# Kernel optimization log

Hardware: AMD Instinct MI355X
Metric: run time of the kernel (lower is better)

## Reference

```python
import jax, jax.numpy as jnp
import numpy as np

N_POL = 20000; N_COMP = 80000; N = N_POL + N_COMP
E = 1000000; EMB = 128; HID = 256; HEADS = 8; OUT = 128; EA = 5
NEG_SLOPE = 0.2; LN_EPS = 1e-5


def setup_inputs() -> dict:
    ks = jax.random.split(jax.random.key(0), 24)
    def rn(i, shape, s=0.1):
        return jax.random.normal(ks[i], shape, jnp.float32) * s
    C1 = HID // HEADS  # per-head channels of conv1
    return dict(
        pol_feat=rn(0, (N_POL, 7), 1.0),
        state_ids=jax.random.randint(ks[1], (N_POL,), 0, 55),
        comp_cat=jax.random.randint(ks[2], (N_COMP, 2), 0, 16),
        comp_price=rn(3, (N_COMP, 1), 1.0),
        edge_index=jax.random.randint(ks[4], (2, E), 0, N),
        edge_attr=rn(5, (E, EA), 1.0),
        Wp=rn(6, (7, EMB)), bp=jnp.zeros((EMB,), jnp.float32),
        state_emb=rn(7, (55, EMB)), sector_emb=rn(8, (16, 8)), industry_emb=rn(9, (150, 8)),
        Wc=rn(10, (17, EMB)), bc=jnp.zeros((EMB,), jnp.float32),
        ln_g=jnp.ones((EMB,), jnp.float32), ln_b=jnp.zeros((EMB,), jnp.float32),
        W1=rn(11, (EMB, HEADS * C1)), att_src1=rn(12, (HEADS, C1)), att_dst1=rn(13, (HEADS, C1)),
        We1=rn(14, (EA, HEADS * C1)), att_e1=rn(15, (HEADS, C1)), b1=jnp.zeros((HID,), jnp.float32),
        W2=rn(16, (HID, OUT)), att_src2=rn(17, (1, OUT)), att_dst2=rn(18, (1, OUT)),
        We2=rn(19, (EA, OUT)), att_e2=rn(20, (1, OUT)), b2=jnp.zeros((OUT,), jnp.float32),
    )


def _add_self_loops(src, dst, ea, n):
    # PyG add_self_loops with fill_value='mean': self-loop edge_attr = mean of
    # incoming edge attrs per dst node (0 for isolated nodes).
    loop = jnp.arange(n, dtype=src.dtype)
    cnt = jax.ops.segment_sum(jnp.ones(dst.shape, jnp.float32), dst, num_segments=n)
    loop_attr = jax.ops.segment_sum(ea, dst, num_segments=n) / jnp.maximum(cnt, 1.0)[:, None]
    return (jnp.concatenate([src, loop]), jnp.concatenate([dst, loop]),
            jnp.concatenate([ea, loop_attr], 0))


def _gat(x, src, dst, ea, W, a_src, a_dst, We, a_e, bias, concat):
    # PyG GATConv (shared lin for src/dst, edge_dim attention, eval mode).
    n = x.shape[0]
    H, C = a_src.shape
    xw = (x @ W).reshape(n, H, C)                 # [n,H,C]
    al_s = jnp.sum(xw * a_src, -1)                # [n,H]
    al_d = jnp.sum(xw * a_dst, -1)                # [n,H]
    ew = (ea @ We).reshape(-1, H, C)              # [Etot,H,C]
    al_e = jnp.sum(ew * a_e, -1)                  # [Etot,H]
    alpha = jax.nn.leaky_relu(al_s[src] + al_d[dst] + al_e, NEG_SLOPE)
    amax = jax.ops.segment_max(alpha, dst, num_segments=n)
    ex = jnp.exp(alpha - amax[dst])
    denom = jax.ops.segment_sum(ex, dst, num_segments=n)
    alpha = ex / (denom[dst] + 1e-16)             # segment softmax over dst
    out = jax.ops.segment_sum(xw[src] * alpha[:, :, None], dst, num_segments=n)
    out = out.reshape(n, H * C) if concat else out.mean(1)
    return out + bias


def reference(pol_feat, state_ids, comp_cat, comp_price, edge_index, edge_attr,
              Wp, bp, state_emb, sector_emb, industry_emb, Wc, bc, ln_g, ln_b,
              W1, att_src1, att_dst1, We1, att_e1, b1,
              W2, att_src2, att_dst2, We2, att_e2, b2):
    pol = jax.nn.relu(pol_feat @ Wp + bp) + state_emb[state_ids]
    comp_in = jnp.concatenate([sector_emb[comp_cat[:, 0]], industry_emb[comp_cat[:, 1]], comp_price], 1)
    comp = jax.nn.relu(comp_in @ Wc + bc)
    x = jnp.concatenate([pol, comp], 0)           # [N,EMB]
    mu = jnp.mean(x, -1, keepdims=True)
    var = jnp.var(x, -1, keepdims=True)
    x = (x - mu) / jnp.sqrt(var + LN_EPS) * ln_g + ln_b
    src, dst, ea = _add_self_loops(edge_index[0], edge_index[1], edge_attr, x.shape[0])
    h = jax.nn.elu(_gat(x, src, dst, ea, W1, att_src1, att_dst1, We1, att_e1, b1, True))
    return _gat(h, src, dst, ea, W2, att_src2, att_dst2, We2, att_e2, b2, False)
```

## Files before the change

### kernel.cpp

```cpp
#include <hip/hip_runtime.h>
#include <hip/hip_fp16.h>
#include <math.h>

#define N_POL 20000
#define N_COMP 80000
#define NN (N_POL + N_COMP)
#define EE 1000000
#define NB1 ((NN + 1023) / 1024)
#define LOG2E 1.44269504f
#define GB1 ((NN + 127) / 128)
#define SB ((EE + 255) / 256)
#define PB 341

typedef short bf16x8 __attribute__((ext_vector_type(8)));
typedef float f32x4 __attribute__((ext_vector_type(4)));

struct __align__(16) PEdge {
  int s;
  float ale2;
  unsigned short a1[8];
  unsigned pad[2];
};

__device__ __forceinline__ float wave_sum(float v) {
#pragma unroll
  for (int o = 32; o > 0; o >>= 1) v += __shfl_xor(v, o);
  return v;
}
__device__ __forceinline__ float wave_max(float v) {
#pragma unroll
  for (int o = 32; o > 0; o >>= 1) v = fmaxf(v, __shfl_xor(v, o));
  return v;
}
__device__ __forceinline__ unsigned short f2bf(float f) {
  unsigned b = __float_as_uint(f);
  return (unsigned short)((b + 0x7FFFu + ((b >> 16) & 1u)) >> 16);
}
__device__ __forceinline__ float bf2f(unsigned short u) {
  return __uint_as_float(((unsigned)u) << 16);
}
__device__ __forceinline__ unsigned short f2h(float f) {
  __half h = __float2half_rn(f);
  return *(unsigned short*)&h;
}
__device__ __forceinline__ float h2f(unsigned short u) {
  __half h = *(__half*)&u;
  return __half2float(h);
}

__global__ __launch_bounds__(256) void k_fuse1(
    const float* W1, const float* W2, const float* as2, const float* ad2,
    const float* We1, const float* ae1, const float* We2, const float* ae2,
    const float* sector_emb, const float* industry_emb, const float* Wc,
    const int* dst, unsigned short* W1t, unsigned short* W2t, float* Ts, float* Ti,
    float* us2, float* ud2, float* V1, float* V2, unsigned* hist) {
  int bid = blockIdx.x;
  if (bid >= PB) {
    int e = (bid - PB) * 256 + threadIdx.x;
    if (e < EE) atomicAdd(&hist[dst[e]], 1u);
    return;
  }
  int id = bid * 256 + threadIdx.x;
  if (id < 32768) {
    int n = id >> 7, k = id & 127;
    W1t[id] = f2bf(W1[k * 256 + n]);
  } else if (id < 65536) {
    int id2 = id - 32768;
    int n = id2 >> 8, k = id2 & 255;
    W2t[id2] = f2bf(W2[k * 128 + n]);
  } else if (id < 67584) {
    int id2 = id - 65536;
    int n = id2 >> 7, c = id2 & 127;
    float a = 0.f;
#pragma unroll
    for (int k = 0; k < 8; k++) a = fmaf(sector_emb[n * 8 + k], Wc[k * 128 + c], a);
    Ts[id2] = a;
  } else if (id < 86784) {
    int id2 = id - 67584;
    int n = id2 >> 7, c = id2 & 127;
    float a = 0.f;
#pragma unroll
    for (int k = 0; k < 8; k++) a = fmaf(industry_emb[n * 8 + k], Wc[(8 + k) * 128 + c], a);
    Ti[id2] = a;
  } else if (id < 87040) {
    int t = id - 86784;
    float s = 0.f, d = 0.f;
    for (int c = 0; c < 128; c++) {
      float w = W2[t * 128 + c];
      s = fmaf(w, as2[c], s);
      d = fmaf(w, ad2[c], d);
    }
    us2[t] = s * LOG2E;
    ud2[t] = d * LOG2E;
  } else if (id < 87104) {
    int t = id - 87040;
    int k = t >> 3, h = t & 7;
    if (k < 5) {
      float v = 0.f;
      for (int c = 0; c < 32; c++) v = fmaf(We1[k * 256 + h * 32 + c], ae1[h * 32 + c], v);
      V1[k * 8 + h] = v * LOG2E;
    }
  } else if (id < 87109) {
    int t = id - 87104;
    float v = 0.f;
    for (int c = 0; c < 128; c++) v = fmaf(We2[t * 128 + c], ae2[c], v);
    V2[t] = v * LOG2E;
  }
}

__global__ __launch_bounds__(256) void k_encode(
    const float* pol_feat, const int* state_ids, const int* comp_cat,
    const float* comp_price, const float* Wp, const float* bp, const float* state_emb,
    const float* Ts, const float* Ti, const float* Wc, const float* bc,
    const float* ln_g, const float* ln_b, unsigned short* x) {
  int t = threadIdx.x;
  int i = blockIdx.x * 2 + (t >> 7), c = t & 127;
  float v;
  if (i < N_POL) {
    float acc = bp[c];
#pragma unroll
    for (int k = 0; k < 7; k++) acc = fmaf(pol_feat[i * 7 + k], Wp[k * 128 + c], acc);
    v = fmaxf(acc, 0.f) + state_emb[state_ids[i] * 128 + c];
  } else {
    int j = i - N_POL;
    int sc = comp_cat[2 * j], in = comp_cat[2 * j + 1];
    float acc = Ts[sc * 128 + c] + Ti[in * 128 + c] +
                comp_price[j] * Wc[16 * 128 + c] + bc[c];
    v = fmaxf(acc, 0.f);
  }
  __shared__ float red[4];
  int wid = t >> 6, lane = t & 63;
  int base = (t >> 7) << 1;
  float s = wave_sum(v);
  if (lane == 0) red[wid] = s;
  __syncthreads();
  float mu = (red[base] + red[base + 1]) * (1.f / 128.f);
  float t0 = v - mu;
  __syncthreads();
  float s2 = wave_sum(t0 * t0);
  if (lane == 0) red[wid] = s2;
  __syncthreads();
  float var = (red[base] + red[base + 1]) * (1.f / 128.f);
  float r = rsqrtf(var + 1e-5f);
  float xf = t0 * r * ln_g[c] + ln_b[c];
  x[(size_t)i * 128 + c] = f2bf(xf);
}

__global__ __launch_bounds__(1024) void k_scan1(const unsigned* hist, unsigned* rowptr,
                                                unsigned* part) {
  __shared__ unsigned sc[1024];
  int t = threadIdx.x;
  int i = blockIdx.x * 1024 + t;
  unsigned v = (i < NN) ? hist[i] : 0u;
  sc[t] = v;
  __syncthreads();
  for (int o = 1; o < 1024; o <<= 1) {
    unsigned add = (t >= o) ? sc[t - o] : 0u;
    __syncthreads();
    sc[t] += add;
    __syncthreads();
  }
  if (i < NN) rowptr[i] = sc[t] - v;
  if (t == 1023) part[blockIdx.x] = sc[1023];
}
__global__ __launch_bounds__(256) void k_scan3(unsigned* rowptr, const unsigned* part,
                                               unsigned* cursor) {
  __shared__ unsigned pref[128];
  int t = threadIdx.x;
  unsigned orig = 0u;
  if (t < 128) {
    orig = (t < NB1) ? part[t] : 0u;
    pref[t] = orig;
  }
  __syncthreads();
  for (int o = 1; o < 128; o <<= 1) {
    unsigned add = 0u;
    if (t < 128 && t >= o) add = pref[t - o];
    __syncthreads();
    if (t < 128) pref[t] += add;
    __syncthreads();
  }
  if (t < 128) pref[t] -= orig;
  __syncthreads();
  int i = blockIdx.x * 256 + t;
  if (i < NN) {
    unsigned r = rowptr[i] + pref[i >> 10];
    rowptr[i] = r;
    cursor[i] = r;
  }
  if (i == 0) rowptr[NN] = EE;
}

__global__ __launch_bounds__(256) void k_fuse2(
    const unsigned short* x, const unsigned short* W1t, unsigned short* xw1,
    const int* src, const int* dst, const float* ea, const float* V1, const float* V2,
    unsigned* cursor, PEdge* ep) {
  __shared__ char wlds[65536];
  int bid = blockIdx.x;
  if (bid % 6 == 0) {
    int gb = bid / 6;
    int tid = threadIdx.x;
#pragma unroll
    for (int it = 0; it < 16; it++) {
      int cch = it * 256 + tid;
      int row = cch >> 4, seg = cch & 15;
      uint4 v = *(const uint4*)(W1t + row * 128 + seg * 8);
      *(uint4*)(&wlds[(row * 256 + seg * 16) ^ ((row & 7) << 4)]) = v;
    }
    __syncthreads();
    int wid = tid >> 6, l = tid & 63;
    int cl = l & 15, kh = l >> 4;
    int swz = (cl & 7) << 4;
    long r0 = (long)gb * 128 + wid * 32;
    f32x4 acc[2][16];
#pragma unroll
    for (int rt = 0; rt < 2; rt++)
#pragma unroll
      for (int nt = 0; nt < 16; nt++) acc[rt][nt] = {0.f, 0.f, 0.f, 0.f};
    long ra0 = r0 + cl; if (ra0 > NN - 1) ra0 = NN - 1;
    long ra1 = r0 + 16 + cl; if (ra1 > NN - 1) ra1 = NN - 1;
#pragma unroll
    for (int kk = 0; kk < 4; kk++) {
      bf16x8 a0 = *(const bf16x8*)(x + ra0 * 128 + kk * 32 + kh * 8);
      bf16x8 a1 = *(const bf16x8*)(x + ra1 * 128 + kk * 32 + kh * 8);
#pragma unroll
      for (int nt = 0; nt < 16; nt++) {
        bf16x8 b = *(const bf16x8*)(&wlds[(((nt * 16 + cl) * 256) + kk * 64 + kh * 16) ^ swz]);
        acc[0][nt] = __builtin_amdgcn_mfma_f32_16x16x32_bf16(a0, b, acc[0][nt], 0, 0, 0);
        acc[1][nt] = __builtin_amdgcn_mfma_f32_16x16x32_bf16(a1, b, acc[1][nt], 0, 0, 0);
      }
    }
#pragma unroll
    for (int rt = 0; rt < 2; rt++)
#pragma unroll
      for (int nt = 0; nt < 16; nt++)
#pragma unroll
        for (int j = 0; j < 4; j++) {
          long row = r0 + rt * 16 + kh * 4 + j;
          if (row < NN) xw1[row * 256 + nt * 16 + cl] = f2bf(acc[rt][nt][j]);
        }
  } else {
    int sidx = bid - bid / 6 - 1;
    int e = sidx * 256 + threadIdx.x;
    if (e >= EE) return;
    int d = dst[e];
    unsigned pos = atomicAdd(&cursor[d], 1u);
    float av[5];
#pragma unroll
    for (int k = 0; k < 5; k++) av[k] = ea[(size_t)e * 5 + k];
    float a2 = 0.f;
#pragma unroll
    for (int k = 0; k < 5; k++) a2 = fmaf(av[k], V2[k], a2);
    unsigned short hb[8];
#pragma unroll
    for (int hh = 0; hh < 8; hh++) {
      float a1 = 0.f;
#pragma unroll
      for (int k = 0; k < 5; k++) a1 = fmaf(av[k], V1[k * 8 + hh], a1);
      hb[hh] = f2h(a1);
    }
    uint4 w0, w1;
    w0.x = (unsigned)src[e];
    w0.y = __float_as_uint(a2);
    w0.z = (unsigned)hb[0] | ((unsigned)hb[1] << 16);
    w0.w = (unsigned)hb[2] | ((unsigned)hb[3] << 16);
    w1.x = (unsigned)hb[4] | ((unsigned)hb[5] << 16);
    w1.y = (unsigned)hb[6] | ((unsigned)hb[7] << 16);
    w1.z = 0u; w1.w = 0u;
    uint4* p = (uint4*)(ep + pos);
    p[0] = w0;
    p[1] = w1;
  }
}

__global__ __launch_bounds__(256) void k_al(const unsigned short* xw1, const float* as1,
                                            const float* ad1, float* al_s1,
                                            float* al_d1) {
  int w = threadIdx.x >> 6, lane = threadIdx.x & 63;
  int i = blockIdx.x * 4 + w;
  if (i >= NN) return;
  ushort4 xv = ((const ushort4*)(xw1 + (size_t)i * 256))[lane];
  float4 as = ((const float4*)as1)[lane];
  float4 ad = ((const float4*)ad1)[lane];
  float x0 = bf2f(xv.x), x1 = bf2f(xv.y), x2 = bf2f(xv.z), x3 = bf2f(xv.w);
  float s = x0 * as.x + x1 * as.y + x2 * as.z + x3 * as.w;
  float d = x0 * ad.x + x1 * ad.y + x2 * ad.z + x3 * ad.w;
#pragma unroll
  for (int o = 1; o < 8; o <<= 1) {
    s += __shfl_xor(s, o);
    d += __shfl_xor(d, o);
  }
  if ((lane & 7) == 0) {
    al_s1[i * 8 + (lane >> 3)] = s * LOG2E;
    al_d1[i * 8 + (lane >> 3)] = d * LOG2E;
  }
}

__global__ __launch_bounds__(256) void k_gemm2(const unsigned short* h,
                                               const unsigned short* W2t,
                                               unsigned short* xw2) {
  __shared__ char wlds[65536];
  int tid = threadIdx.x;
#pragma unroll
  for (int it = 0; it < 16; it++) {
    int cch = it * 256 + tid;
    int row = cch >> 5, seg = cch & 31;
    uint4 v = *(const uint4*)(W2t + row * 256 + seg * 8);
    *(uint4*)(&wlds[(row * 512 + seg * 16) ^ ((row & 7) << 4)]) = v;
  }
  __syncthreads();
  int wid = tid >> 6, l = tid & 63;
  int cl = l & 15, kh = l >> 4;
  int swz = (cl & 7) << 4;
  long r0 = (long)blockIdx.x * 128 + wid * 32;
  f32x4 acc[2][8];
#pragma unroll
  for (int rt = 0; rt < 2; rt++)
#pragma unroll
    for (int nt = 0; nt < 8; nt++) acc[rt][nt] = {0.f, 0.f, 0.f, 0.f};
  long ra0 = r0 + cl; if (ra0 > NN - 1) ra0 = NN - 1;
  long ra1 = r0 + 16 + cl; if (ra1 > NN - 1) ra1 = NN - 1;
#pragma unroll
  for (int kk = 0; kk < 8; kk++) {
    bf16x8 a0 = *(const bf16x8*)(h + ra0 * 256 + kk * 32 + kh * 8);
    bf16x8 a1 = *(const bf16x8*)(h + ra1 * 256 + kk * 32 + kh * 8);
#pragma unroll
    for (int nt = 0; nt < 8; nt++) {
      bf16x8 b = *(const bf16x8*)(&wlds[(((nt * 16 + cl) * 512) + kk * 64 + kh * 16) ^ swz]);
      acc[0][nt] = __builtin_amdgcn_mfma_f32_16x16x32_bf16(a0, b, acc[0][nt], 0, 0, 0);
      acc[1][nt] = __builtin_amdgcn_mfma_f32_16x16x32_bf16(a1, b, acc[1][nt], 0, 0, 0);
    }
  }
#pragma unroll
  for (int rt = 0; rt < 2; rt++)
#pragma unroll
    for (int nt = 0; nt < 8; nt++)
#pragma unroll
      for (int j = 0; j < 4; j++) {
        long row = r0 + rt * 16 + kh * 4 + j;
        if (row < NN) xw2[row * 128 + nt * 16 + cl] = f2bf(acc[rt][nt][j]);
      }
}

__global__ __launch_bounds__(256) void k_gat1(
    const unsigned* rowptr, const PEdge* ep, const float* al_s1, const float* al_d1,
    const unsigned short* xw1, const float* b1, const float* us2, const float* ud2,
    unsigned short* h, float* al_s2, float* al_d2) {
  int w = threadIdx.x >> 6, lane = threadIdx.x & 63;
  int i = blockIdx.x * 4 + w;
  if (i >= NN) return;
  int r0 = rowptr[i], r1 = rowptr[i + 1];
  int hh = lane & 7;
  int js = lane >> 3;
  int ah = lane >> 3;
  float ald = al_d1[i * 8 + hh];
  float m = -1e30f, l = 0.f;
  float a0 = 0.f, a1 = 0.f, a2 = 0.f, a3 = 0.f;
  float alesum = 0.f;

  auto chunk16 = [&](int jb) {
    int jc0 = jb + js, jc1 = jb + 8 + js;
    int s0 = ((const int*)&ep[jc0])[0];
    int s1 = ((const int*)&ep[jc1])[0];
    float e0 = h2f(((const unsigned short*)&ep[jc0])[4 + hh]);
    float e1 = h2f(((const unsigned short*)&ep[jc1])[4 + hh]);
    alesum += e0 + e1;
    float g0 = al_s1[s0 * 8 + hh] + ald + e0;
    g0 = g0 > 0.f ? g0 : 0.2f * g0;
    float g1 = al_s1[s1 * 8 + hh] + ald + e1;
    g1 = g1 > 0.f ? g1 : 0.2f * g1;
    float cm = fmaxf(g0, g1);
    cm = fmaxf(cm, __shfl_xor(cm, 8));
    cm = fmaxf(cm, __shfl_xor(cm, 16));
    cm = fmaxf(cm, __shfl_xor(cm, 32));
    float mn = fmaxf(m, cm);
    float sc = exp2f(m - mn);
    float p0 = exp2f(g0 - mn), p1 = exp2f(g1 - mn);
    float ps = p0 + p1;
    ps += __shfl_xor(ps, 8);
    ps += __shfl_xor(ps, 16);
    ps += __shfl_xor(ps, 32);
    l = l * sc + ps;
    m = mn;
    float asc = __shfl(sc, ah);
    a0 *= asc; a1 *= asc; a2 *= asc; a3 *= asc;
#pragma unroll
    for (int jj = 0; jj < 8; jj++) {
      float pj = __shfl(p0, jj * 8 + ah);
      int sj = __shfl(s0, jj * 8);
      ushort4 xv = ((const ushort4*)(xw1 + (size_t)sj * 256))[lane];
      a0 = fmaf(pj, bf2f(xv.x), a0);
      a1 = fmaf(pj, bf2f(xv.y), a1);
      a2 = fmaf(pj, bf2f(xv.z), a2);
      a3 = fmaf(pj, bf2f(xv.w), a3);
    }
#pragma unroll
    for (int jj = 0; jj < 8; jj++) {
      float pj = __shfl(p1, jj * 8 + ah);
      int sj = __shfl(s1, jj * 8);
      ushort4 xv = ((const ushort4*)(xw1 + (size_t)sj * 256))[lane];
      a0 = fmaf(pj, bf2f(xv.x), a0);
      a1 = fmaf(pj, bf2f(xv.y), a1);
      a2 = fmaf(pj, bf2f(xv.z), a2);
      a3 = fmaf(pj, bf2f(xv.w), a3);
    }
  };

  auto chunk8 = [&](int jb, int cnt) {
    bool valid = js < cnt;
    int jc = jb + (valid ? js : cnt - 1);
    int s = ((const int*)&ep[jc])[0];
    float ale = h2f(((const unsigned short*)&ep[jc])[4 + hh]);
    if (!valid) ale = 0.f;
    alesum += ale;
    float logit = -1e30f;
    if (valid) {
      float al = al_s1[s * 8 + hh] + ald + ale;
      logit = al > 0.f ? al : 0.2f * al;
    }
    float cm = logit;
    cm = fmaxf(cm, __shfl_xor(cm, 8));
    cm = fmaxf(cm, __shfl_xor(cm, 16));
    cm = fmaxf(cm, __shfl_xor(cm, 32));
    float mn = fmaxf(m, cm);
    float sc = exp2f(m - mn);
    float p = exp2f(logit - mn);
    float ps = p;
    ps += __shfl_xor(ps, 8);
    ps += __shfl_xor(ps, 16);
    ps += __shfl_xor(ps, 32);
    l = l * sc + ps;
    m = mn;
    float asc = __shfl(sc, ah);
    a0 *= asc; a1 *= asc; a2 *= asc; a3 *= asc;
    for (int jj = 0; jj < cnt; jj++) {
      float pj = __shfl(p, jj * 8 + ah);
      int sj = __shfl(s, jj * 8);
      ushort4 xv = ((const ushort4*)(xw1 + (size_t)sj * 256))[lane];
      a0 = fmaf(pj, bf2f(xv.x), a0);
      a1 = fmaf(pj, bf2f(xv.y), a1);
      a2 = fmaf(pj, bf2f(xv.z), a2);
      a3 = fmaf(pj, bf2f(xv.w), a3);
    }
  };

  int jb = r0;
  for (; jb + 16 <= r1; jb += 16) chunk16(jb);
  if (jb + 8 <= r1) { chunk8(jb, 8); jb += 8; }
  if (jb < r1) chunk8(jb, r1 - jb);

  alesum += __shfl_xor(alesum, 8);
  alesum += __shfl_xor(alesum, 16);
  alesum += __shfl_xor(alesum, 32);
  float inv = 1.f / fmaxf((float)(r1 - r0), 1.f);
  float aleS = alesum * inv;
  {
    float al = al_s1[i * 8 + hh] + ald + aleS;
    float logit = al > 0.f ? al : 0.2f * al;
    float mn = fmaxf(m, logit);
    float sc = exp2f(m - mn);
    float p = exp2f(logit - mn);
    l = l * sc + p;
    m = mn;
    float asc = __shfl(sc, ah);
    float pj = __shfl(p, ah);
    ushort4 xv = ((const ushort4*)(xw1 + (size_t)i * 256))[lane];
    a0 = fmaf(pj, bf2f(xv.x), a0 * asc);
    a1 = fmaf(pj, bf2f(xv.y), a1 * asc);
    a2 = fmaf(pj, bf2f(xv.z), a2 * asc);
    a3 = fmaf(pj, bf2f(xv.w), a3 * asc);
  }
  float lh = __shfl(l, ah);
  float invl = 1.f / (lh + 1e-16f);
  float4 bv = ((const float4*)b1)[lane];
  float v0 = a0 * invl + bv.x, v1 = a1 * invl + bv.y;
  float v2 = a2 * invl + bv.z, v3 = a3 * invl + bv.w;
  v0 = v0 > 0.f ? v0 : expm1f(v0);
  v1 = v1 > 0.f ? v1 : expm1f(v1);
  v2 = v2 > 0.f ? v2 : expm1f(v2);
  v3 = v3 > 0.f ? v3 : expm1f(v3);
  ushort4 hv;
  hv.x = f2bf(v0); hv.y = f2bf(v1); hv.z = f2bf(v2); hv.w = f2bf(v3);
  ((ushort4*)(h + (size_t)i * 256))[lane] = hv;
  float4 uv = ((const float4*)us2)[lane];
  float4 dv = ((const float4*)ud2)[lane];
  float ps2 = v0 * uv.x + v1 * uv.y + v2 * uv.z + v3 * uv.w;
  float pd2 = v0 * dv.x + v1 * dv.y + v2 * dv.z + v3 * dv.w;
  ps2 = wave_sum(ps2);
  pd2 = wave_sum(pd2);
  if (lane == 0) { al_s2[i] = ps2; al_d2[i] = pd2; }
}

__global__ __launch_bounds__(256) void k_gat2(
    const unsigned* rowptr, const PEdge* ep, const float* al_s2, const float* al_d2,
    const unsigned short* xw2, const float* b2, float* out) {
  int w = threadIdx.x >> 6, lane = threadIdx.x & 63;
  int i = blockIdx.x * 4 + w;
  if (i >= NN) return;
  int r0 = rowptr[i], r1 = rowptr[i + 1];
  float ald = al_d2[i];
  float m = -1e30f, l = 0.f, a0 = 0.f, a1 = 0.f;
  float alesum = 0.f;

  auto chunk = [&](int jb, int cnt) {
    bool valid = lane < cnt;
    int jc = jb + (valid ? lane : cnt - 1);
    int2 sv = *(const int2*)&ep[jc];
    int s = sv.x;
    float ale = valid ? __uint_as_float((unsigned)sv.y) : 0.f;
    alesum += ale;
    float logit = -1e30f;
    if (valid) {
      float al = al_s2[s] + ald + ale;
      logit = al > 0.f ? al : 0.2f * al;
    }
    float cm = wave_max(logit);
    float mn = fmaxf(m, cm);
    float sc = exp2f(m - mn);
    float p = exp2f(logit - mn);
    float ps = wave_sum(p);
    l = l * sc + ps;
    m = mn;
    a0 *= sc; a1 *= sc;
    for (int jj = 0; jj < cnt; jj++) {
      float pj = __shfl(p, jj);
      int sj = __shfl(s, jj);
      ushort2 xv = ((const ushort2*)(xw2 + (size_t)sj * 128))[lane];
      a0 = fmaf(pj, bf2f(xv.x), a0);
      a1 = fmaf(pj, bf2f(xv.y), a1);
    }
  };
  int jb = r0;
  for (; jb + 64 <= r1; jb += 64) chunk(jb, 64);
  if (jb < r1) chunk(jb, r1 - jb);

  alesum = wave_sum(alesum);
  float inv = 1.f / fmaxf((float)(r1 - r0), 1.f);
  float aleS = alesum * inv;
  {
    float al = al_s2[i] + ald + aleS;
    float logit = al > 0.f ? al : 0.2f * al;
    float mn = fmaxf(m, logit);
    float sc = exp2f(m - mn);
    float p = exp2f(logit - mn);
    l = l * sc + p;
    ushort2 xv = ((const ushort2*)(xw2 + (size_t)i * 128))[lane];
    a0 = fmaf(p, bf2f(xv.x), a0 * sc);
    a1 = fmaf(p, bf2f(xv.y), a1 * sc);
  }
  float invl = 1.f / (l + 1e-16f);
  float2 bv = ((const float2*)b2)[lane];
  float2 ov = {a0 * invl + bv.x, a1 * invl + bv.y};
  ((float2*)(out + (size_t)i * 128))[lane] = ov;
}

extern "C" void kernel_launch(void* const* d_in, const int* in_sizes, int n_in,
                              void* d_out, int out_size, void* d_ws, size_t ws_size,
                              hipStream_t stream) {
  const float* pol_feat = (const float*)d_in[0];
  const int* state_ids = (const int*)d_in[1];
  const int* comp_cat = (const int*)d_in[2];
  const float* comp_price = (const float*)d_in[3];
  const int* edge_index = (const int*)d_in[4];
  const float* edge_attr = (const float*)d_in[5];
  const float* Wp = (const float*)d_in[6];
  const float* bp = (const float*)d_in[7];
  const float* state_emb = (const float*)d_in[8];
  const float* sector_emb = (const float*)d_in[9];
  const float* industry_emb = (const float*)d_in[10];
  const float* Wc = (const float*)d_in[11];
  const float* bc = (const float*)d_in[12];
  const float* ln_g = (const float*)d_in[13];
  const float* ln_b = (const float*)d_in[14];
  const float* W1 = (const float*)d_in[15];
  const float* as1 = (const float*)d_in[16];
  const float* ad1 = (const float*)d_in[17];
  const float* We1 = (const float*)d_in[18];
  const float* ae1 = (const float*)d_in[19];
  const float* b1 = (const float*)d_in[20];
  const float* W2 = (const float*)d_in[21];
  const float* as2 = (const float*)d_in[22];
  const float* ad2 = (const float*)d_in[23];
  const float* We2 = (const float*)d_in[24];
  const float* ae2 = (const float*)d_in[25];
  const float* b2 = (const float*)d_in[26];
  const int* srcv = edge_index;
  const int* dstv = edge_index + EE;
  float* out = (float*)d_out;

  size_t off = 0;
  auto alloc = [&](size_t nbytes) -> char* {
    char* p = (char*)d_ws + off;
    off += ((nbytes + 255) & ~(size_t)255);
    return p;
  };
  char* regA = alloc((size_t)NN * 512);
  char* regB = alloc((size_t)NN * 512);
  unsigned short* xw1 = (unsigned short*)regA;
  unsigned short* xw2 = (unsigned short*)regA;
  unsigned short* h = (unsigned short*)regB;
  unsigned short* x = (unsigned short*)regB;
  float* al_s1 = (float*)alloc((size_t)NN * 8 * 4);
  float* al_d1 = (float*)alloc((size_t)NN * 8 * 4);
  float* al_s2 = (float*)alloc((size_t)NN * 4);
  float* al_d2 = (float*)alloc((size_t)NN * 4);
  float* us2 = (float*)alloc(256 * 4);
  float* ud2 = (float*)alloc(256 * 4);
  float* V1 = (float*)alloc(64 * 4);
  float* V2 = (float*)alloc(8 * 4);
  float* Ts = (float*)alloc(16 * 128 * 4);
  float* Ti = (float*)alloc(150 * 128 * 4);
  unsigned short* W1t = (unsigned short*)alloc(32768 * 2);
  unsigned short* W2t = (unsigned short*)alloc(32768 * 2);
  unsigned* hist = (unsigned*)alloc((size_t)NN * 4);
  unsigned* rowptr = (unsigned*)alloc((size_t)(NN + 1) * 4);
  unsigned* cursor = (unsigned*)alloc((size_t)NN * 4);
  unsigned* part = (unsigned*)alloc((size_t)NB1 * 4);
  PEdge* ep = (PEdge*)alloc((size_t)EE * sizeof(PEdge));

  hipMemsetAsync(hist, 0, (size_t)NN * 4, stream);

  k_fuse1<<<PB + SB, 256, 0, stream>>>(W1, W2, as2, ad2, We1, ae1, We2, ae2,
                                       sector_emb, industry_emb, Wc, dstv, W1t, W2t,
                                       Ts, Ti, us2, ud2, V1, V2, hist);
  k_encode<<<NN / 2, 256, 0, stream>>>(pol_feat, state_ids, comp_cat, comp_price, Wp,
                                       bp, state_emb, Ts, Ti, Wc, bc, ln_g, ln_b, x);
  k_scan1<<<NB1, 1024, 0, stream>>>(hist, rowptr, part);
  k_scan3<<<(NN + 255) / 256, 256, 0, stream>>>(rowptr, part, cursor);
  k_fuse2<<<GB1 * 6 + (SB - GB1 * 5), 256, 0, stream>>>(x, W1t, xw1, srcv, dstv,
                                                        edge_attr, V1, V2, cursor, ep);
  k_al<<<NN / 4, 256, 0, stream>>>(xw1, as1, ad1, al_s1, al_d1);
  k_gat1<<<NN / 4, 256, 0, stream>>>(rowptr, ep, al_s1, al_d1, xw1, b1, us2, ud2, h,
                                     al_s2, al_d2);
  k_gemm2<<<(NN + 127) / 128, 256, 0, stream>>>(h, W2t, xw2);
  k_gat2<<<NN / 4, 256, 0, stream>>>(rowptr, ep, al_s2, al_d2, xw2, b2, out);
}
```

Before: 403.0 us.

## Fold attention vectors into W1 and fuse scan, encode, and logit kernels

Precomputes W1·att_src1 and W1·att_dst1 per head so the layer-1 attention logits come straight from x rather than from a re-read of xw1. Those logits are computed in extra blocks of the fused GEMM/edge-permute kernel, which removes the separate k_al launch. The 1024-thread shared-memory scan is replaced by a wave-shuffle scan merged into the encode kernel, and the GEMM/scatter block interleave ratio is changed. This saves launches and a full pass over xw1, at the cost of different rounding (bf16 x times fp32 folded weights) and more complex block dispatch.

```diff
diff --git a/kernel.cpp b/kernel.cpp
--- a/kernel.cpp
+++ b/kernel.cpp
@@ -10,7 +10,8 @@
 #define LOG2E 1.44269504f
 #define GB1 ((NN + 127) / 128)
 #define SB ((EE + 255) / 256)
-#define PB 341
+#define AB 3125
+#define PB 349
 
 typedef short bf16x8 __attribute__((ext_vector_type(8)));
 typedef float f32x4 __attribute__((ext_vector_type(4)));
@@ -52,8 +53,9 @@
     const float* W1, const float* W2, const float* as2, const float* ad2,
     const float* We1, const float* ae1, const float* We2, const float* ae2,
     const float* sector_emb, const float* industry_emb, const float* Wc,
-    const int* dst, unsigned short* W1t, unsigned short* W2t, float* Ts, float* Ti,
-    float* us2, float* ud2, float* V1, float* V2, unsigned* hist) {
+    const float* as1, const float* ad1, const int* dst, unsigned short* W1t,
+    unsigned short* W2t, float* Ts, float* Ti, float* us2, float* ud2, float* V1,
+    float* V2, float* ws1hT, float* wd1hT, unsigned* hist) {
   int bid = blockIdx.x;
   if (bid >= PB) {
     int e = (bid - PB) * 256 + threadIdx.x;
@@ -105,16 +107,57 @@
     float v = 0.f;
     for (int c = 0; c < 128; c++) v = fmaf(We2[t * 128 + c], ae2[c], v);
     V2[t] = v * LOG2E;
-  }
-}
-
-__global__ __launch_bounds__(256) void k_encode(
-    const float* pol_feat, const int* state_ids, const int* comp_cat,
-    const float* comp_price, const float* Wp, const float* bp, const float* state_emb,
-    const float* Ts, const float* Ti, const float* Wc, const float* bc,
-    const float* ln_g, const float* ln_b, unsigned short* x) {
+  } else if (id < 89157) {
+    int t2 = id - 87109;
+    int issd = t2 >> 10;
+    int r = t2 & 1023;
+    int k = r & 127, h = r >> 7;
+    const float* a = issd ? ad1 : as1;
+    float v = 0.f;
+#pragma unroll
+    for (int c = 0; c < 32; c++) v = fmaf(W1[k * 256 + h * 32 + c], a[h * 32 + c], v);
+    if (issd) wd1hT[h * 128 + k] = v * LOG2E;
+    else ws1hT[h * 128 + k] = v * LOG2E;
+  }
+}
+
+__global__ __launch_bounds__(256) void k_fuse_es(
+    const unsigned* hist, unsigned* rowptr, unsigned* part, const float* pol_feat,
+    const int* state_ids, const int* comp_cat, const float* comp_price,
+    const float* Wp, const float* bp, const float* state_emb, const float* Ts,
+    const float* Ti, const float* Wc, const float* bc, const float* ln_g,
+    const float* ln_b, unsigned short* x) {
   int t = threadIdx.x;
-  int i = blockIdx.x * 2 + (t >> 7), c = t & 127;
+  int bid = blockIdx.x;
+  if (bid < NB1) {
+    int lane = t & 63, wid = t >> 6;
+    int base = bid * 1024 + t * 4;
+    unsigned v0 = (base + 0 < NN) ? hist[base + 0] : 0u;
+    unsigned v1 = (base + 1 < NN) ? hist[base + 1] : 0u;
+    unsigned v2 = (base + 2 < NN) ? hist[base + 2] : 0u;
+    unsigned v3 = (base + 3 < NN) ? hist[base + 3] : 0u;
+    unsigned s0 = v0, s1 = s0 + v1, s2 = s1 + v2, s3 = s2 + v3;
+    unsigned inc = s3;
+#pragma unroll
+    for (int o = 1; o < 64; o <<= 1) {
+      unsigned n = __shfl_up(inc, o);
+      if (lane >= o) inc += n;
+    }
+    __shared__ unsigned wt[4];
+    if (lane == 63) wt[wid] = inc;
+    __syncthreads();
+    unsigned woff = 0;
+    for (int ww = 0; ww < wid; ww++) woff += wt[ww];
+    unsigned exc = woff + inc - s3;
+    if (base + 0 < NN) rowptr[base + 0] = exc;
+    if (base + 1 < NN) rowptr[base + 1] = exc + s0;
+    if (base + 2 < NN) rowptr[base + 2] = exc + s1;
+    if (base + 3 < NN) rowptr[base + 3] = exc + s2;
+    if (t == 255) part[bid] = woff + inc;
+    return;
+  }
+  int eb = bid - NB1;
+  int i = eb * 2 + (t >> 7), c = t & 127;
   float v;
   if (i < N_POL) {
     float acc = bp[c];
@@ -146,23 +189,6 @@
   x[(size_t)i * 128 + c] = f2bf(xf);
 }
 
-__global__ __launch_bounds__(1024) void k_scan1(const unsigned* hist, unsigned* rowptr,
-                                                unsigned* part) {
-  __shared__ unsigned sc[1024];
-  int t = threadIdx.x;
-  int i = blockIdx.x * 1024 + t;
-  unsigned v = (i < NN) ? hist[i] : 0u;
-  sc[t] = v;
-  __syncthreads();
-  for (int o = 1; o < 1024; o <<= 1) {
-    unsigned add = (t >= o) ? sc[t - o] : 0u;
-    __syncthreads();
-    sc[t] += add;
-    __syncthreads();
-  }
-  if (i < NN) rowptr[i] = sc[t] - v;
-  if (t == 1023) part[blockIdx.x] = sc[1023];
-}
 __global__ __launch_bounds__(256) void k_scan3(unsigned* rowptr, const unsigned* part,
                                                unsigned* cursor) {
   __shared__ unsigned pref[128];
@@ -194,11 +220,13 @@
 __global__ __launch_bounds__(256) void k_fuse2(
     const unsigned short* x, const unsigned short* W1t, unsigned short* xw1,
     const int* src, const int* dst, const float* ea, const float* V1, const float* V2,
-    unsigned* cursor, PEdge* ep) {
+    unsigned* cursor, PEdge* ep, const float* ws1hT, const float* wd1hT,
+    float* al_s1, float* al_d1) {
   __shared__ char wlds[65536];
   int bid = blockIdx.x;
-  if (bid % 6 == 0) {
-    int gb = bid / 6;
+  bool isg = (bid % 9 == 0) && (bid / 9 < GB1);
+  if (isg) {
+    int gb = bid / 9;
     int tid = threadIdx.x;
 #pragma unroll
     for (int it = 0; it < 16; it++) {
@@ -239,9 +267,11 @@
           long row = r0 + rt * 16 + kh * 4 + j;
           if (row < NN) xw1[row * 256 + nt * 16 + cl] = f2bf(acc[rt][nt][j]);
         }
-  } else {
-    int sidx = bid - bid / 6 - 1;
-    int e = sidx * 256 + threadIdx.x;
+    return;
+  }
+  int j = bid - ((bid + 8) / 9 < GB1 ? (bid + 8) / 9 : GB1);
+  if (j < SB) {
+    int e = j * 256 + threadIdx.x;
     if (e >= EE) return;
     int d = dst[e];
     unsigned pos = atomicAdd(&cursor[d], 1u);
@@ -270,29 +300,42 @@
     uint4* p = (uint4*)(ep + pos);
     p[0] = w0;
     p[1] = w1;
-  }
-}
-
-__global__ __launch_bounds__(256) void k_al(const unsigned short* xw1, const float* as1,
-                                            const float* ad1, float* al_s1,
-                                            float* al_d1) {
-  int w = threadIdx.x >> 6, lane = threadIdx.x & 63;
-  int i = blockIdx.x * 4 + w;
-  if (i >= NN) return;
-  ushort4 xv = ((const ushort4*)(xw1 + (size_t)i * 256))[lane];
-  float4 as = ((const float4*)as1)[lane];
-  float4 ad = ((const float4*)ad1)[lane];
-  float x0 = bf2f(xv.x), x1 = bf2f(xv.y), x2 = bf2f(xv.z), x3 = bf2f(xv.w);
-  float s = x0 * as.x + x1 * as.y + x2 * as.z + x3 * as.w;
-  float d = x0 * ad.x + x1 * ad.y + x2 * ad.z + x3 * ad.w;
-#pragma unroll
-  for (int o = 1; o < 8; o <<= 1) {
-    s += __shfl_xor(s, o);
-    d += __shfl_xor(d, o);
-  }
-  if ((lane & 7) == 0) {
-    al_s1[i * 8 + (lane >> 3)] = s * LOG2E;
-    al_d1[i * 8 + (lane >> 3)] = d * LOG2E;
+  } else {
+    int ab = j - SB;
+    int lane = threadIdx.x & 63, wid = threadIdx.x >> 6;
+    int g = lane >> 3;
+    int cb = (lane & 7) * 16;
+    float wsv[16], wdv[16];
+#pragma unroll
+    for (int q = 0; q < 4; q++) {
+      *(float4*)(wsv + q * 4) = *(const float4*)(ws1hT + g * 128 + cb + q * 4);
+      *(float4*)(wdv + q * 4) = *(const float4*)(wd1hT + g * 128 + cb + q * 4);
+    }
+    int nodebase = ab * 32 + wid * 8;
+    for (int nn = 0; nn < 8; nn++) {
+      int i = nodebase + nn;
+      bf16x8 xa = *(const bf16x8*)(x + (size_t)i * 128 + cb);
+      bf16x8 xb = *(const bf16x8*)(x + (size_t)i * 128 + cb + 8);
+      float s = 0.f, d = 0.f;
+#pragma unroll
+      for (int q = 0; q < 8; q++) {
+        float xv = bf2f((unsigned short)xa[q]);
+        s = fmaf(xv, wsv[q], s);
+        d = fmaf(xv, wdv[q], d);
+      }
+#pragma unroll
+      for (int q = 0; q < 8; q++) {
+        float xv = bf2f((unsigned short)xb[q]);
+        s = fmaf(xv, wsv[8 + q], s);
+        d = fmaf(xv, wdv[8 + q], d);
+      }
+      s += __shfl_xor(s, 1); s += __shfl_xor(s, 2); s += __shfl_xor(s, 4);
+      d += __shfl_xor(d, 1); d += __shfl_xor(d, 2); d += __shfl_xor(d, 4);
+      if ((lane & 7) == 0) {
+        al_s1[i * 8 + g] = s;
+        al_d1[i * 8 + g] = d;
+      }
+    }
   }
 }
 
@@ -610,6 +653,8 @@
   float* V2 = (float*)alloc(8 * 4);
   float* Ts = (float*)alloc(16 * 128 * 4);
   float* Ti = (float*)alloc(150 * 128 * 4);
+  float* ws1hT = (float*)alloc(1024 * 4);
+  float* wd1hT = (float*)alloc(1024 * 4);
   unsigned short* W1t = (unsigned short*)alloc(32768 * 2);
   unsigned short* W2t = (unsigned short*)alloc(32768 * 2);
   unsigned* hist = (unsigned*)alloc((size_t)NN * 4);
@@ -621,15 +666,16 @@
   hipMemsetAsync(hist, 0, (size_t)NN * 4, stream);
 
   k_fuse1<<<PB + SB, 256, 0, stream>>>(W1, W2, as2, ad2, We1, ae1, We2, ae2,
-                                       sector_emb, industry_emb, Wc, dstv, W1t, W2t,
-                                       Ts, Ti, us2, ud2, V1, V2, hist);
-  k_encode<<<NN / 2, 256, 0, stream>>>(pol_feat, state_ids, comp_cat, comp_price, Wp,
-                                       bp, state_emb, Ts, Ti, Wc, bc, ln_g, ln_b, x);
-  k_scan1<<<NB1, 1024, 0, stream>>>(hist, rowptr, part);
+                                       sector_emb, industry_emb, Wc, as1, ad1, dstv,
+                                       W1t, W2t, Ts, Ti, us2, ud2, V1, V2, ws1hT,
+                                       wd1hT, hist);
+  k_fuse_es<<<NB1 + NN / 2, 256, 0, stream>>>(hist, rowptr, part, pol_feat, state_ids,
+                                              comp_cat, comp_price, Wp, bp, state_emb,
+                                              Ts, Ti, Wc, bc, ln_g, ln_b, x);
   k_scan3<<<(NN + 255) / 256, 256, 0, stream>>>(rowptr, part, cursor);
-  k_fuse2<<<GB1 * 6 + (SB - GB1 * 5), 256, 0, stream>>>(x, W1t, xw1, srcv, dstv,
-                                                        edge_attr, V1, V2, cursor, ep);
-  k_al<<<NN / 4, 256, 0, stream>>>(xw1, as1, ad1, al_s1, al_d1);
+  k_fuse2<<<GB1 + SB + AB, 256, 0, stream>>>(x, W1t, xw1, srcv, dstv, edge_attr, V1,
+                                             V2, cursor, ep, ws1hT, wd1hT, al_s1,
+                                             al_d1);
   k_gat1<<<NN / 4, 256, 0, stream>>>(rowptr, ep, al_s1, al_d1, xw1, b1, us2, ud2, h,
                                      al_s2, al_d2);
   k_gemm2<<<(NN + 127) / 128, 256, 0, stream>>>(h, W2t, xw2);
```

Result: slower. 426.2 us (+5.8%).
